# Optimization experiments

Hardware: AMD Instinct MI355X
Metric: run time of the kernel (lower is better)

## Reference

```python
import jax, jax.numpy as jnp
import numpy as np

BIG = 1.0e6  # sentinel 'infinite' 1D distance (BIG**2 = 1e12 is safely finite in fp32)


def _edt_sq(zero_mask):
    """Exact squared Euclidean distance transform to nearest True in zero_mask.

    Two-pass separable exact EDT (matches scipy.ndimage.distance_transform_edt):
      pass 1: 1-D distance along W via forward/backward cummax scans
      pass 2: min-plus over H: D2[i,j] = min_k g2[k,j] + (i-k)^2
    zero_mask: [H, W] bool (True where the source array equals 0).
    """
    H, W = zero_mask.shape
    col = jnp.arange(W, dtype=jnp.float32)
    # index of last zero to the left / first zero to the right
    last = jax.lax.cummax(jnp.where(zero_mask, col, -BIG), axis=1)
    nxt = -jax.lax.cummax(jnp.where(zero_mask, -col, -BIG), axis=1, reverse=True)
    g = jnp.minimum(jnp.minimum(col - last, nxt - col), BIG)  # [H, W] 1-D dist
    g2 = g * g
    row = jnp.arange(H, dtype=jnp.float32)
    sq = (row[:, None] - row[None, :]) ** 2  # [H, H]
    # D2[i, j] = min_k g2[k, j] + (i - k)^2  -- exact 2-D squared EDT
    return jnp.min(g2[None, :, :] + sq[:, :, None], axis=1)


def _distance_map(mask):
    """Signed distance map: EDT(mask) - EDT(1 - mask); zeros if mask empty."""
    pos = jnp.sqrt(_edt_sq(mask == 0))   # dist of foreground px to nearest background
    neg = jnp.sqrt(_edt_sq(mask != 0))   # dist of background px to nearest foreground
    d = pos - neg
    return jnp.where(mask.sum() == 0, jnp.zeros_like(d), d)


def boundary_loss(pred, target):
    B, C, H, W = pred.shape
    masks = target.reshape(B * C, H, W)
    # sequence over B*C to keep the [H,H,W] min-plus intermediate per-image
    dmaps = jax.lax.map(_distance_map, masks).reshape(B, C, H, W)
    # sum_c mean_{b,h,w}(sig(pred_c)*d_c) / C  ==  overall mean
    return jnp.mean(jax.nn.sigmoid(pred) * dmaps)


def setup_inputs() -> dict:
    key = jax.random.key(0)
    k1, k2 = jax.random.split(key)
    pred = jax.random.normal(k1, (8, 3, 256, 256), dtype=jnp.float32)
    target = jax.random.randint(k2, (8, 3, 256, 256), 0, 2, dtype=jnp.int32)
    return {"pred": pred, "target": target}


def reference(pred, target):
    return boundary_loss(pred, target)
```

## Files before the change

kernel.cpp:

```cpp
#include <hip/hip_runtime.h>
#include <math.h>

#define NIMG 24
#define H    256
#define W    256
#define NPIX (H * W)
#define NROWS (NIMG * H)
#define CPB  16
#define NBLK2 (NIMG * (W / CPB))
#define LDP2 17
#define BIGI 1000000
#define CAPS 1024

__global__ __launch_bounds__(256)
void edt_rows_kernel(const int* __restrict__ tgt,
                     short* __restrict__ f,
                     float* __restrict__ out) {
    if (blockIdx.x == 0 && threadIdx.x == 0) out[0] = 0.0f;

    const int t    = threadIdx.x;
    const int rloc = t >> 4;
    const int ck   = t & 15;
    const int row  = blockIdx.x * 16 + rloc;
    const int j0   = ck << 4;
    const int base = (row << 8) + j0;

    __shared__ unsigned long long m[16][4];

    const int4* rp = (const int4*)(tgt + base);
    const int4 v0 = rp[0], v1 = rp[1], v2 = rp[2], v3 = rp[3];
    const int prevv = (ck > 0) ? tgt[base - 1] : 0;

    int va[16];
    *(int4*)&va[0]  = v0;  *(int4*)&va[4]  = v1;
    *(int4*)&va[8]  = v2;  *(int4*)&va[12] = v3;

    unsigned int bits = 0;
    {
        bool pc = (prevv != 0);
#pragma unroll
        for (int i = 0; i < 16; ++i) {
            const bool c = (va[i] != 0);
            if (c != pc) bits |= (1u << i);
            pc = c;
        }
        if (ck == 0) bits &= ~1u;
    }
    ((unsigned short*)m)[(rloc << 4) + ck] = (unsigned short)bits;
    __syncthreads();

    const unsigned long long M0 = m[rloc][0], M1 = m[rloc][1];
    const unsigned long long M2 = m[rloc][2], M3 = m[rloc][3];
    const int wlo = ck >> 2;
    const int blo = (ck & 3) << 4;
    const int bhi = blo + 16;

    const unsigned long long pm  = blo ? ((1ULL << blo) - 1ULL) : 0ULL;
    const unsigned long long lm0 = (wlo > 0) ? ~0ULL : pm;
    const unsigned long long lm1 = (wlo > 1) ? ~0ULL : ((wlo == 1) ? pm : 0ULL);
    const unsigned long long lm2 = (wlo > 2) ? ~0ULL : ((wlo == 2) ? pm : 0ULL);
    const unsigned long long lm3 = (wlo == 3) ? pm : 0ULL;
    int last = -BIGI;
    {
        unsigned long long x;
        x = M0 & lm0; if (x) last = 63 - __builtin_clzll(x);
        x = M1 & lm1; if (x) last = 127 - __builtin_clzll(x);
        x = M2 & lm2; if (x) last = 191 - __builtin_clzll(x);
        x = M3 & lm3; if (x) last = 255 - __builtin_clzll(x);
    }

    const unsigned long long sm  = (bhi == 64) ? 0ULL : ~((1ULL << bhi) - 1ULL);
    const unsigned long long hm0 = (wlo == 0) ? sm : 0ULL;
    const unsigned long long hm1 = (wlo < 1) ? ~0ULL : ((wlo == 1) ? sm : 0ULL);
    const unsigned long long hm2 = (wlo < 2) ? ~0ULL : ((wlo == 2) ? sm : 0ULL);
    const unsigned long long hm3 = (wlo < 3) ? ~0ULL : sm;
    int nxt_hi = BIGI;
    {
        unsigned long long x;
        x = M3 & hm3; if (x) nxt_hi = 192 + __builtin_ctzll(x);
        x = M2 & hm2; if (x) nxt_hi = 128 + __builtin_ctzll(x);
        x = M1 & hm1; if (x) nxt_hi =  64 + __builtin_ctzll(x);
        x = M0 & hm0; if (x) nxt_hi =       __builtin_ctzll(x);
    }

    short os[16];
    unsigned int rem = bits;
#pragma unroll
    for (int i = 0; i < 16; ++i) {
        const int j = j0 + i;
        if (rem & 1u) last = j;
        rem >>= 1;
        const int n  = rem ? (j + 1 + __builtin_ctz(rem)) : nxt_hi;
        const int dp = j - last + 1;
        const int dn = n - j;
        int g = dp < dn ? dp : dn;
        g = (g < BIGI) ? g : CAPS;
        os[i] = (short)((va[i] != 0) ? g : -g);
    }

    int pk[8];
#pragma unroll
    for (int i = 0; i < 8; ++i)
        pk[i] = (int)((unsigned short)os[2 * i] |
                      ((unsigned int)(unsigned short)os[2 * i + 1] << 16));
    int4* op = (int4*)(f + base);
    op[0] = make_int4(pk[0], pk[1], pk[2], pk[3]);
    op[1] = make_int4(pk[4], pk[5], pk[6], pk[7]);
}

__global__ __launch_bounds__(512)
void edt_cols_kernel(const short* __restrict__ f,
                     const float* __restrict__ pred,
                     float* __restrict__ out) {
    const int bid  = blockIdx.x;
    const int img  = bid >> 4;
    const int j0   = (bid & 15) << 4;
    const int t    = threadIdx.x;
    const int lane = t & 63;
    const int wid  = t >> 6;

    __shared__ float sf[H][LDP2];
    __shared__ double wsum[8];
    __shared__ int nonempty;
    if (t == 0) nonempty = 0;
    __syncthreads();

    {
        const int row = t >> 1;
        const int q   = (t & 1) << 3;
        const int4 rv = *(const int4*)(f + (img << 16) + (row << 8) + j0 + q);
        const short* sv = (const short*)&rv;
        bool ne = false;
#pragma unroll
        for (int j = 0; j < 8; ++j) {
            const int v = sv[j];
            ne = ne || (v != -CAPS);
            float g = (float)v;
            if (v == CAPS)  g =  1.0e6f;
            if (v == -CAPS) g = -1.0e6f;
            sf[row][q + j] = g;
        }
        if (ne) nonempty = 1;
    }

    const int c  = t & 15;
    const int r0 = (t >> 4) << 3;
    float pf[8];
#pragma unroll
    for (int ii = 0; ii < 8; ++ii)
        pf[ii] = pred[(img << 16) + ((r0 + ii) << 8) + j0 + c];

    __syncthreads();
    const int flag = nonempty;

    double acc = 0.0;
#pragma unroll
    for (int ii = 0; ii < 8; ++ii) {
        const int i = r0 + ii;
        const float fv = sf[i][c];
        const bool  m  = fv > 0.0f;
        const float sgn = m ? 1.0f : -1.0f;
        const float gi = fabsf(fv);
        const int  gii = (int)gi;
        int lo = i - gii; lo = lo > 0 ? lo : 0;
        int hi = i + gii; hi = hi < (H - 1) ? hi : (H - 1);

        float dm = 3.0e38f;
        float dk = (float)(i - lo);
        for (int k = lo; k <= hi; ++k) {
            const float g = fmaxf(sgn * sf[k][c], 0.0f);
            dm = fminf(dm, g * g + dk * dk);
            dk -= 1.0f;
        }

        float d = m ? sqrtf(dm) : -sqrtf(dm);
        if (!flag) d = 0.0f;
        const float sig = 1.0f / (1.0f + expf(-pf[ii]));
        acc += (double)sig * (double)d;
    }

#pragma unroll
    for (int off = 32; off > 0; off >>= 1) acc += __shfl_down(acc, off, 64);
    if (lane == 0) wsum[wid] = acc;
    __syncthreads();
    if (t == 0) {
        double s = 0.0;
#pragma unroll
        for (int w = 0; w < 8; ++w) s += wsum[w];
        atomicAdd(out, (float)(s * (1.0 / (double)(NIMG * NPIX))));
    }
}

extern "C" void kernel_launch(void* const* d_in, const int* in_sizes, int n_in,
                              void* d_out, int out_size, void* d_ws, size_t ws_size,
                              hipStream_t stream) {
    const float* pred = (const float*)d_in[0];
    const int*   tgt  = (const int*)d_in[1];
    float* out = (float*)d_out;

    short* fbuf = (short*)d_ws;

    edt_rows_kernel<<<384, 256, 0, stream>>>(tgt, fbuf, out);
    edt_cols_kernel<<<NBLK2, 512, 0, stream>>>(fbuf, pred, out);
}
```

Before: 23.34 us.

## Fuse row and column EDT passes into one kernel with partial-sum finalize

Merges the row-wise 1-D distance pass into the column min-plus kernel. Each block recomputes the row transition bitmasks for its whole image in shared memory, so the intermediate short buffer no longer goes through global memory. Blocks are mapped so an image's column groups stay on the same XCD, which should let repeated target reads hit L2. The float atomicAdd is replaced by per-block double partials plus a small finalize kernel. In exchange, each block reads the full 256x256 target image, which is 16x redundant global traffic, and blocks drop to 256 threads with 16 rows per thread.

```diff
diff --git a/kernel.cpp b/kernel.cpp
--- a/kernel.cpp
+++ b/kernel.cpp
@@ -5,161 +5,135 @@
 #define H    256
 #define W    256
 #define NPIX (H * W)
-#define NROWS (NIMG * H)
 #define CPB  16
-#define NBLK2 (NIMG * (W / CPB))
-#define LDP2 17
+#define GRPS (W / CPB)
+#define NBLK (NIMG * GRPS)
+#define LDP  17
 #define BIGI 1000000
-#define CAPS 1024
 
 __global__ __launch_bounds__(256)
-void edt_rows_kernel(const int* __restrict__ tgt,
-                     short* __restrict__ f,
-                     float* __restrict__ out) {
-    if (blockIdx.x == 0 && threadIdx.x == 0) out[0] = 0.0f;
+void boundary_main_kernel(const int* __restrict__ tgt,
+                          const float* __restrict__ pred,
+                          double* __restrict__ partials) {
+    const int bid = blockIdx.x;
+    const int xcd = bid & 7;
+    const int k   = bid >> 3;
+    const int img = xcd * 3 + (k % 3);
+    const int grp = k / 3;
+    const int j0  = grp << 4;
+    const int t   = threadIdx.x;
+    const int lane = t & 63;
+    const int wid  = t >> 6;
+    const int ibase = img << 16;
 
-    const int t    = threadIdx.x;
-    const int rloc = t >> 4;
-    const int ck   = t & 15;
-    const int row  = blockIdx.x * 16 + rloc;
-    const int j0   = ck << 4;
-    const int base = (row << 8) + j0;
+    __shared__ unsigned long long m[H][4];
+    __shared__ unsigned short sgnb[H];
+    __shared__ float sf[H][LDP];
+    __shared__ double wsum[4];
+    __shared__ int nonempty;
+    if (t == 0) nonempty = 0;
+    __syncthreads();
 
-    __shared__ unsigned long long m[16][4];
+    int anynz = 0;
+#pragma unroll 2
+    for (int s = 0; s < 16; ++s) {
+        const int task = (s << 8) + t;
+        const int row  = task >> 4;
+        const int ck   = task & 15;
+        const int base = ibase + (row << 8) + (ck << 4);
+        const int4* rp = (const int4*)(tgt + base);
+        const int4 v0 = rp[0], v1 = rp[1], v2 = rp[2], v3 = rp[3];
+        int va[16];
+        *(int4*)&va[0]  = v0;  *(int4*)&va[4]  = v1;
+        *(int4*)&va[8]  = v2;  *(int4*)&va[12] = v3;
+        const int prevv = ck ? tgt[base - 1] : 0;
 
-    const int4* rp = (const int4*)(tgt + base);
-    const int4 v0 = rp[0], v1 = rp[1], v2 = rp[2], v3 = rp[3];
-    const int prevv = (ck > 0) ? tgt[base - 1] : 0;
-
-    int va[16];
-    *(int4*)&va[0]  = v0;  *(int4*)&va[4]  = v1;
-    *(int4*)&va[8]  = v2;  *(int4*)&va[12] = v3;
-
-    unsigned int bits = 0;
-    {
+        unsigned int bits = 0, sbits = 0;
         bool pc = (prevv != 0);
 #pragma unroll
         for (int i = 0; i < 16; ++i) {
             const bool c = (va[i] != 0);
             if (c != pc) bits |= (1u << i);
+            if (c) sbits |= (1u << i);
             pc = c;
         }
         if (ck == 0) bits &= ~1u;
+        anynz |= sbits;
+        ((unsigned short*)m)[task] = (unsigned short)bits;
+        if (ck == grp) sgnb[row] = (unsigned short)sbits;
     }
-    ((unsigned short*)m)[(rloc << 4) + ck] = (unsigned short)bits;
-    __syncthreads();
-
-    const unsigned long long M0 = m[rloc][0], M1 = m[rloc][1];
-    const unsigned long long M2 = m[rloc][2], M3 = m[rloc][3];
-    const int wlo = ck >> 2;
-    const int blo = (ck & 3) << 4;
-    const int bhi = blo + 16;
-
-    const unsigned long long pm  = blo ? ((1ULL << blo) - 1ULL) : 0ULL;
-    const unsigned long long lm0 = (wlo > 0) ? ~0ULL : pm;
-    const unsigned long long lm1 = (wlo > 1) ? ~0ULL : ((wlo == 1) ? pm : 0ULL);
-    const unsigned long long lm2 = (wlo > 2) ? ~0ULL : ((wlo == 2) ? pm : 0ULL);
-    const unsigned long long lm3 = (wlo == 3) ? pm : 0ULL;
-    int last = -BIGI;
-    {
-        unsigned long long x;
-        x = M0 & lm0; if (x) last = 63 - __builtin_clzll(x);
-        x = M1 & lm1; if (x) last = 127 - __builtin_clzll(x);
-        x = M2 & lm2; if (x) last = 191 - __builtin_clzll(x);
-        x = M3 & lm3; if (x) last = 255 - __builtin_clzll(x);
-    }
-
-    const unsigned long long sm  = (bhi == 64) ? 0ULL : ~((1ULL << bhi) - 1ULL);
-    const unsigned long long hm0 = (wlo == 0) ? sm : 0ULL;
-    const unsigned long long hm1 = (wlo < 1) ? ~0ULL : ((wlo == 1) ? sm : 0ULL);
-    const unsigned long long hm2 = (wlo < 2) ? ~0ULL : ((wlo == 2) ? sm : 0ULL);
-    const unsigned long long hm3 = (wlo < 3) ? ~0ULL : sm;
-    int nxt_hi = BIGI;
-    {
-        unsigned long long x;
-        x = M3 & hm3; if (x) nxt_hi = 192 + __builtin_ctzll(x);
-        x = M2 & hm2; if (x) nxt_hi = 128 + __builtin_ctzll(x);
-        x = M1 & hm1; if (x) nxt_hi =  64 + __builtin_ctzll(x);
-        x = M0 & hm0; if (x) nxt_hi =       __builtin_ctzll(x);
-    }
-
-    short os[16];
-    unsigned int rem = bits;
-#pragma unroll
-    for (int i = 0; i < 16; ++i) {
-        const int j = j0 + i;
-        if (rem & 1u) last = j;
-        rem >>= 1;
-        const int n  = rem ? (j + 1 + __builtin_ctz(rem)) : nxt_hi;
-        const int dp = j - last + 1;
-        const int dn = n - j;
-        int g = dp < dn ? dp : dn;
-        g = (g < BIGI) ? g : CAPS;
-        os[i] = (short)((va[i] != 0) ? g : -g);
-    }
-
-    int pk[8];
-#pragma unroll
-    for (int i = 0; i < 8; ++i)
-        pk[i] = (int)((unsigned short)os[2 * i] |
-                      ((unsigned int)(unsigned short)os[2 * i + 1] << 16));
-    int4* op = (int4*)(f + base);
-    op[0] = make_int4(pk[0], pk[1], pk[2], pk[3]);
-    op[1] = make_int4(pk[4], pk[5], pk[6], pk[7]);
-}
-
-__global__ __launch_bounds__(512)
-void edt_cols_kernel(const short* __restrict__ f,
-                     const float* __restrict__ pred,
-                     float* __restrict__ out) {
-    const int bid  = blockIdx.x;
-    const int img  = bid >> 4;
-    const int j0   = (bid & 15) << 4;
-    const int t    = threadIdx.x;
-    const int lane = t & 63;
-    const int wid  = t >> 6;
-
-    __shared__ float sf[H][LDP2];
-    __shared__ double wsum[8];
-    __shared__ int nonempty;
-    if (t == 0) nonempty = 0;
+    if (anynz) nonempty = 1;
     __syncthreads();
 
     {
-        const int row = t >> 1;
-        const int q   = (t & 1) << 3;
-        const int4 rv = *(const int4*)(f + (img << 16) + (row << 8) + j0 + q);
-        const short* sv = (const short*)&rv;
-        bool ne = false;
+        const int row = t;
+        const unsigned long long M0 = m[row][0], M1 = m[row][1];
+        const unsigned long long M2 = m[row][2], M3 = m[row][3];
+        const int wlo = grp >> 2;
+        const int blo = (grp & 3) << 4;
+        const int bhi = blo + 16;
+
+        const unsigned long long pm  = blo ? ((1ULL << blo) - 1ULL) : 0ULL;
+        const unsigned long long lm0 = (wlo > 0) ? ~0ULL : pm;
+        const unsigned long long lm1 = (wlo > 1) ? ~0ULL : ((wlo == 1) ? pm : 0ULL);
+        const unsigned long long lm2 = (wlo > 2) ? ~0ULL : ((wlo == 2) ? pm : 0ULL);
+        const unsigned long long lm3 = (wlo == 3) ? pm : 0ULL;
+        int last = -BIGI;
+        {
+            unsigned long long x;
+            x = M0 & lm0; if (x) last = 63 - __builtin_clzll(x);
+            x = M1 & lm1; if (x) last = 127 - __builtin_clzll(x);
+            x = M2 & lm2; if (x) last = 191 - __builtin_clzll(x);
+            x = M3 & lm3; if (x) last = 255 - __builtin_clzll(x);
+        }
+        const unsigned long long sm  = (bhi == 64) ? 0ULL : ~((1ULL << bhi) - 1ULL);
+        const unsigned long long hm0 = (wlo == 0) ? sm : 0ULL;
+        const unsigned long long hm1 = (wlo < 1) ? ~0ULL : ((wlo == 1) ? sm : 0ULL);
+        const unsigned long long hm2 = (wlo < 2) ? ~0ULL : ((wlo == 2) ? sm : 0ULL);
+        const unsigned long long hm3 = (wlo < 3) ? ~0ULL : sm;
+        int nxt_hi = BIGI;
+        {
+            unsigned long long x;
+            x = M3 & hm3; if (x) nxt_hi = 192 + __builtin_ctzll(x);
+            x = M2 & hm2; if (x) nxt_hi = 128 + __builtin_ctzll(x);
+            x = M1 & hm1; if (x) nxt_hi =  64 + __builtin_ctzll(x);
+            x = M0 & hm0; if (x) nxt_hi =       __builtin_ctzll(x);
+        }
+
+        const unsigned long long Mw =
+            (wlo == 0) ? M0 : (wlo == 1) ? M1 : (wlo == 2) ? M2 : M3;
+        unsigned int rem = (unsigned int)((Mw >> blo) & 0xFFFFULL);
+        const unsigned int sb = sgnb[row];
 #pragma unroll
-        for (int j = 0; j < 8; ++j) {
-            const int v = sv[j];
-            ne = ne || (v != -CAPS);
-            float g = (float)v;
-            if (v == CAPS)  g =  1.0e6f;
-            if (v == -CAPS) g = -1.0e6f;
-            sf[row][q + j] = g;
+        for (int i = 0; i < 16; ++i) {
+            const int j = j0 + i;
+            if (rem & 1u) last = j;
+            rem >>= 1;
+            const int n  = rem ? (j + 1 + __builtin_ctz(rem)) : nxt_hi;
+            const int dp = j - last + 1;
+            const int dn = n - j;
+            const int g  = dp < dn ? dp : dn;
+            const float gf = (g < BIGI) ? (float)g : 1.0e6f;
+            sf[row][i] = ((sb >> i) & 1u) ? gf : -gf;
         }
-        if (ne) nonempty = 1;
     }
-
-    const int c  = t & 15;
-    const int r0 = (t >> 4) << 3;
-    float pf[8];
-#pragma unroll
-    for (int ii = 0; ii < 8; ++ii)
-        pf[ii] = pred[(img << 16) + ((r0 + ii) << 8) + j0 + c];
-
     __syncthreads();
     const int flag = nonempty;
 
+    const int c  = t & 15;
+    const int r0 = (t >> 4) << 4;
+    float pf[16];
+#pragma unroll
+    for (int ii = 0; ii < 16; ++ii)
+        pf[ii] = pred[ibase + ((r0 + ii) << 8) + j0 + c];
+
     double acc = 0.0;
-#pragma unroll
-    for (int ii = 0; ii < 8; ++ii) {
+#pragma unroll 4
+    for (int ii = 0; ii < 16; ++ii) {
         const int i = r0 + ii;
         const float fv = sf[i][c];
-        const bool  m  = fv > 0.0f;
-        const float sgn = m ? 1.0f : -1.0f;
+        const bool  m2 = fv > 0.0f;
+        const float sgn = m2 ? 1.0f : -1.0f;
         const float gi = fabsf(fv);
         const int  gii = (int)gi;
         int lo = i - gii; lo = lo > 0 ? lo : 0;
@@ -167,13 +141,13 @@
 
         float dm = 3.0e38f;
         float dk = (float)(i - lo);
-        for (int k = lo; k <= hi; ++k) {
-            const float g = fmaxf(sgn * sf[k][c], 0.0f);
+        for (int kk = lo; kk <= hi; ++kk) {
+            const float g = fmaxf(sgn * sf[kk][c], 0.0f);
             dm = fminf(dm, g * g + dk * dk);
             dk -= 1.0f;
         }
 
-        float d = m ? sqrtf(dm) : -sqrtf(dm);
+        float d = m2 ? sqrtf(dm) : -sqrtf(dm);
         if (!flag) d = 0.0f;
         const float sig = 1.0f / (1.0f + expf(-pf[ii]));
         acc += (double)sig * (double)d;
@@ -183,12 +157,18 @@
     for (int off = 32; off > 0; off >>= 1) acc += __shfl_down(acc, off, 64);
     if (lane == 0) wsum[wid] = acc;
     __syncthreads();
-    if (t == 0) {
-        double s = 0.0;
+    if (t == 0) partials[bid] = (wsum[0] + wsum[1]) + (wsum[2] + wsum[3]);
+}
+
+__global__ void finalize_kernel(const double* __restrict__ partials,
+                                float* __restrict__ out) {
+    const int t = threadIdx.x;
+    double a = 0.0;
 #pragma unroll
-        for (int w = 0; w < 8; ++w) s += wsum[w];
-        atomicAdd(out, (float)(s * (1.0 / (double)(NIMG * NPIX))));
-    }
+    for (int s = 0; s < NBLK / 64; ++s) a += partials[t + (s << 6)];
+#pragma unroll
+    for (int off = 32; off > 0; off >>= 1) a += __shfl_down(a, off, 64);
+    if (t == 0) out[0] = (float)(a / (double)(NIMG * NPIX));
 }
 
 extern "C" void kernel_launch(void* const* d_in, const int* in_sizes, int n_in,
@@ -198,8 +178,8 @@
     const int*   tgt  = (const int*)d_in[1];
     float* out = (float*)d_out;
 
-    short* fbuf = (short*)d_ws;
+    double* partials = (double*)d_ws;
 
-    edt_rows_kernel<<<384, 256, 0, stream>>>(tgt, fbuf, out);
-    edt_cols_kernel<<<NBLK2, 512, 0, stream>>>(fbuf, pred, out);
+    boundary_main_kernel<<<NBLK, 256, 0, stream>>>(tgt, pred, partials);
+    finalize_kernel<<<1, 64, 0, stream>>>(partials, out);
 }
```

Result: slower. 33.09 us (+41.8%).
